# Performance work log

Measured on AMD Instinct MI355X. Metric: run time of the kernel, lower is better.

The kernel has to match this reference:

```python
import jax, jax.numpy as jnp
import numpy as np


def setup_inputs() -> dict:
    key = jax.random.key(0)
    k1, k2, k3, k4 = jax.random.split(key, 4)
    B, S, d_in, d_out = 4, 2048, 1024, 1024
    x = jax.random.normal(k1, (B, S, d_in), dtype=jnp.float32)
    # torch nn.Linear weight is [d_out, d_in]; we store transposed [d_in, d_out]
    Wq = jax.random.normal(k2, (d_in, d_out), dtype=jnp.float32) * (1.0 / np.sqrt(d_in))
    Wk = jax.random.normal(k3, (d_in, d_out), dtype=jnp.float32) * (1.0 / np.sqrt(d_in))
    Wv = jax.random.normal(k4, (d_in, d_out), dtype=jnp.float32) * (1.0 / np.sqrt(d_in))
    return {"x": x, "Wq": Wq, "Wk": Wk, "Wv": Wv}


def reference(x, Wq, Wk, Wv):
    # x: [B, S, d_in]
    B, S, d_in = x.shape
    q = jnp.einsum("bsd,de->bse", x, Wq)
    k = jnp.einsum("bsd,de->bse", x, Wk)
    v = jnp.einsum("bsd,de->bse", x, Wv)
    scores = jnp.einsum("bqe,bke->bqk", q, k)  # [B, S, S]
    causal = jnp.triu(jnp.ones((S, S), dtype=bool), k=1)  # True above diagonal
    scores = jnp.where(causal[None, :, :], -jnp.inf, scores)
    # NOTE: original scales by sqrt(d_in), not sqrt(d_out)
    scale = jnp.asarray(1.0 / np.sqrt(d_in), dtype=scores.dtype)
    weights = jax.nn.softmax(scores * scale, axis=-1)
    # dropout p=0.0 -> identity
    return jnp.einsum("bqk,bke->bqe", weights, v)
```

## Files before the change

kernel.cpp:

```cpp
#include <hip/hip_runtime.h>
#include <hip/hip_bf16.h>

typedef __attribute__((ext_vector_type(8))) short short8;
typedef __attribute__((ext_vector_type(4))) short short4_t;
typedef __attribute__((ext_vector_type(4))) float f32x4;
typedef unsigned short ushort_t;

__device__ __forceinline__ ushort_t f2bf(float f) {
    union { __hip_bfloat16 h; ushort_t u; } c;
    c.h = __float2bfloat16(f);
    return c.u;
}

__device__ __forceinline__ void gload16(const ushort_t* g, ushort_t* l) {
    __builtin_amdgcn_global_load_lds(
        (const __attribute__((address_space(1))) void*)g,
        (__attribute__((address_space(3))) void*)l, 16, 0, 0);
}

__global__ __launch_bounds__(256) void k_prep(const float* __restrict__ x,
                                              const float* __restrict__ Wq,
                                              const float* __restrict__ Wk,
                                              const float* __restrict__ Wv,
                                              ushort_t* __restrict__ xb,
                                              ushort_t* __restrict__ Wqb,
                                              ushort_t* __restrict__ Wkb,
                                              ushort_t* __restrict__ Wvt) {
    const int bz = blockIdx.z;
    const int t = threadIdx.y * 32 + threadIdx.x;
    if (bz == 3) {
        size_t base = ((size_t)(blockIdx.y * 32 + blockIdx.x) * 256 + t) * 8;
#pragma unroll
        for (int p = 0; p < 4; ++p) {
            size_t idx = base + (size_t)p * 2097152;
            float4 a = *(const float4*)(x + idx);
            float4 b = *(const float4*)(x + idx + 4);
            short8 o;
            o[0] = (short)f2bf(a.x); o[1] = (short)f2bf(a.y);
            o[2] = (short)f2bf(a.z); o[3] = (short)f2bf(a.w);
            o[4] = (short)f2bf(b.x); o[5] = (short)f2bf(b.y);
            o[6] = (short)f2bf(b.z); o[7] = (short)f2bf(b.w);
            *(short8*)(xb + idx) = o;
        }
        return;
    }
    if (bz < 2) {
        const float* src = bz ? Wk : Wq;
        ushort_t* dst = bz ? Wkb : Wqb;
        size_t idx = ((size_t)(blockIdx.y * 32 + blockIdx.x) * 256 + t) * 4;
        float4 a = *(const float4*)(src + idx);
        short4_t o;
        o[0] = (short)f2bf(a.x); o[1] = (short)f2bf(a.y);
        o[2] = (short)f2bf(a.z); o[3] = (short)f2bf(a.w);
        *(short4_t*)(dst + idx) = o;
        return;
    }
    __shared__ float tile[32][33];
    int tx = threadIdx.x, ty = threadIdx.y;
    int d0 = blockIdx.y * 32, e0 = blockIdx.x * 32;
#pragma unroll
    for (int i = 0; i < 32; i += 8)
        tile[ty + i][tx] = Wv[(size_t)(d0 + ty + i) * 1024 + e0 + tx];
    __syncthreads();
#pragma unroll
    for (int i = 0; i < 32; i += 8)
        Wvt[(size_t)(e0 + ty + i) * 1024 + d0 + tx] = f2bf(tile[tx][ty + i]);
}

template <int MODE>
__global__ __launch_bounds__(256) void k_gemm(const ushort_t* __restrict__ Abase,
                                              const ushort_t* __restrict__ Bbase,
                                              void* __restrict__ Cbase,
                                              ushort_t* __restrict__ Vt) {
    int bm, bn, bz;
    const ushort_t* A;
    const ushort_t* B;
    if constexpr (MODE == 3) {
        bm = blockIdx.x; bn = blockIdx.y; bz = 0;
        A = Abase; B = Bbase;
    } else {
        bm = blockIdx.x; bn = blockIdx.y; bz = blockIdx.z;
        A = Abase;
        B = Bbase + (size_t)bz * 1048576;
    }
    const int lda = 1024, ldb = 1024, nk = 32;

    constexpr int SMEM_ELEMS = (MODE == 0) ? (128 * 130) : 8192;
    __shared__ ushort_t smem[SMEM_ELEMS];
    ushort_t* As = smem;
    ushort_t* Bs = smem + 4096;

    const int tid = threadIdx.x;
    const int l = tid & 63, wid = tid >> 6;
    const int wr = (wid >> 1) * 64, wc = (wid & 1) * 64;
    const int lr = l & 15, kc = (l >> 4) * 8;

    const int srow = tid >> 2, skb = (tid & 3) * 8;
    const ushort_t* ag = A + (size_t)(bm * 128 + srow) * lda + skb;
    const ushort_t* bg = B + (size_t)(bn * 128 + srow) * ldb + skb;
    const size_t a64 = (size_t)64 * lda, b64 = (size_t)64 * ldb;
    ushort_t* al = As + tid * 8;
    ushort_t* bl = Bs + tid * 8;

    f32x4 zero = {0.f, 0.f, 0.f, 0.f};
    f32x4 acc[4][4];
#pragma unroll
    for (int m = 0; m < 4; ++m)
#pragma unroll
        for (int n = 0; n < 4; ++n) acc[m][n] = zero;

    for (int ks = 0; ks < nk; ++ks) {
        __syncthreads();
        gload16(ag, al);
        gload16(ag + a64, al + 2048);
        gload16(bg, bl);
        gload16(bg + b64, bl + 2048);
        ag += 32; bg += 32;
        __syncthreads();

        short8 a[4], b[4];
#pragma unroll
        for (int m = 0; m < 4; ++m)
            a[m] = *(const short8*)&As[(wr + m * 16 + lr) * 32 + kc];
#pragma unroll
        for (int n = 0; n < 4; ++n)
            b[n] = *(const short8*)&Bs[(wc + n * 16 + lr) * 32 + kc];
#pragma unroll
        for (int m = 0; m < 4; ++m)
#pragma unroll
            for (int n = 0; n < 4; ++n)
                acc[m][n] = __builtin_amdgcn_mfma_f32_16x16x32_bf16(a[m], b[n], acc[m][n], 0, 0, 0);
    }

    const int rbase = (l >> 4) * 4;
    const int cbase = l & 15;

    if constexpr (MODE == 0) {
        if (bz == 1) {
            __syncthreads();
#pragma unroll
            for (int m = 0; m < 4; ++m)
#pragma unroll
                for (int n = 0; n < 4; ++n) {
                    int col = wc + n * 16 + cbase;
                    int row0 = wr + m * 16 + rbase;
#pragma unroll
                    for (int r = 0; r < 4; ++r)
                        smem[col * 130 + row0 + r] = f2bf(acc[m][n][r]);
                }
            __syncthreads();
            const int e = tid >> 1, jh = (tid & 1) * 64;
            const int b = bm >> 4, j0 = (bm * 128) & 2047;
            ushort_t* dst = Vt + (size_t)b * 2097152 +
                            (size_t)(bn * 128 + e) * 2048 + j0 + jh;
            const ushort_t* src = smem + e * 130 + jh;
#pragma unroll
            for (int c = 0; c < 8; ++c)
                *(short8*)(dst + c * 8) = *(const short8*)(src + c * 8);
            return;
        }
    }

#pragma unroll
    for (int m = 0; m < 4; ++m) {
#pragma unroll
        for (int n = 0; n < 4; ++n) {
            int col = wc + n * 16 + cbase;
            int gcol = bn * 128 + col;
#pragma unroll
            for (int r = 0; r < 4; ++r) {
                int grow = bm * 128 + wr + m * 16 + rbase + r;
                ushort_t* C = (ushort_t*)Cbase;
                C[(size_t)grow * 1024 + gcol] = f2bf(acc[m][n][r]);
            }
        }
    }
}

template <int MODE>
__global__ __launch_bounds__(256) void k_gemm64(const ushort_t* __restrict__ Abase,
                                                const ushort_t* __restrict__ Bbase,
                                                void* __restrict__ Cbase) {
    int bm, bn;
    const int bz = blockIdx.z;
    const ushort_t* A;
    const ushort_t* B;
    int lda, ldb, nk;
    if constexpr (MODE == 1) {
        int x = blockIdx.x;
        bm = (int)((sqrtf(4.f * x + 1.f) - 1.f) * 0.5f);
        while ((bm + 1) * (bm + 2) <= x) ++bm;
        while (bm * (bm + 1) > x) --bm;
        bn = x - bm * (bm + 1);
        A = Abase + (size_t)bz * 2048 * 1024; lda = 1024;
        B = Bbase + (size_t)bz * 2048 * 1024; ldb = 1024;
        nk = 32;
    } else {
        int xr = blockIdx.x;
        bm = (xr & 1) ? (15 - (xr >> 1)) : (xr >> 1);
        bn = blockIdx.y;
        A = Abase + (size_t)bz * 2048 * 2048; lda = 2048;
        B = Bbase + (size_t)bz * 1024 * 2048; ldb = 2048;
        nk = (bm + 1) * 4;
    }

    __shared__ ushort_t As[128 * 32];
    __shared__ ushort_t Bs[64 * 32];
    __shared__ float rsh[128];

    const int tid = threadIdx.x;
    const int l = tid & 63, wid = tid >> 6;
    const int wr = (wid >> 1) * 64, wc = (wid & 1) * 32;
    const int lr = l & 15, kc = (l >> 4) * 8;

    const int srow = tid >> 2, skb = (tid & 3) * 8;
    const ushort_t* ag = A + (size_t)(bm * 128 + srow) * lda + skb;
    const ushort_t* bg = B + (size_t)(bn * 64 + srow) * ldb + skb;
    const size_t a64 = (size_t)64 * lda;
    ushort_t* al = As + tid * 8;
    ushort_t* bl = Bs + tid * 8;

    f32x4 zero = {0.f, 0.f, 0.f, 0.f};
    f32x4 acc[4][2];
#pragma unroll
    for (int m = 0; m < 4; ++m) { acc[m][0] = zero; acc[m][1] = zero; }

    f32x4 rs[4];
    short8 ones;
#pragma unroll
    for (int e = 0; e < 8; ++e) ones[e] = (short)0x3F80;
#pragma unroll
    for (int m = 0; m < 4; ++m) rs[m] = zero;

    for (int ks = 0; ks < nk; ++ks) {
        __syncthreads();
        gload16(ag, al);
        gload16(ag + a64, al + 2048);
        gload16(bg, bl);
        ag += 32; bg += 32;
        __syncthreads();

        short8 a[4], b[2];
#pragma unroll
        for (int m = 0; m < 4; ++m)
            a[m] = *(const short8*)&As[(wr + m * 16 + lr) * 32 + kc];
#pragma unroll
        for (int n = 0; n < 2; ++n)
            b[n] = *(const short8*)&Bs[(wc + n * 16 + lr) * 32 + kc];
#pragma unroll
        for (int m = 0; m < 4; ++m)
#pragma unroll
            for (int n = 0; n < 2; ++n)
                acc[m][n] = __builtin_amdgcn_mfma_f32_16x16x32_bf16(a[m], b[n], acc[m][n], 0, 0, 0);
        if constexpr (MODE == 2) {
            if (wc == 0) {
#pragma unroll
                for (int m = 0; m < 4; ++m)
                    rs[m] = __builtin_amdgcn_mfma_f32_16x16x32_bf16(a[m], ones, rs[m], 0, 0, 0);
            }
        }
    }

    const int rbase = (l >> 4) * 4;
    const int cbase = l & 15;

    if constexpr (MODE == 1) {
        ushort_t* C = (ushort_t*)Cbase + (size_t)bz * 2048 * 2048;
#pragma unroll
        for (int m = 0; m < 4; ++m)
#pragma unroll
            for (int n = 0; n < 2; ++n) {
                int gcol = bn * 64 + wc + n * 16 + cbase;
#pragma unroll
                for (int r = 0; r < 4; ++r) {
                    int grow = bm * 128 + wr + m * 16 + rbase + r;
                    ushort_t pv = (gcol <= grow) ? f2bf(__expf(acc[m][n][r] * 0.03125f))
                                                 : (ushort_t)0;
                    C[(size_t)grow * 2048 + gcol] = pv;
                }
            }
    } else {
        if (wc == 0 && lr == 0) {
#pragma unroll
            for (int m = 0; m < 4; ++m)
#pragma unroll
                for (int r = 0; r < 4; ++r)
                    rsh[wr + m * 16 + rbase + r] = rs[m][r];
        }
        __syncthreads();
        float inv[4][4];
#pragma unroll
        for (int m = 0; m < 4; ++m)
#pragma unroll
            for (int r = 0; r < 4; ++r)
                inv[m][r] = 1.0f / rsh[wr + m * 16 + rbase + r];
        float* C = (float*)Cbase + (size_t)bz * 2048 * 1024;
#pragma unroll
        for (int m = 0; m < 4; ++m)
#pragma unroll
            for (int n = 0; n < 2; ++n) {
                int gcol = bn * 64 + wc + n * 16 + cbase;
#pragma unroll
                for (int r = 0; r < 4; ++r) {
                    int grow = bm * 128 + wr + m * 16 + rbase + r;
                    C[(size_t)grow * 1024 + gcol] = acc[m][n][r] * inv[m][r];
                }
            }
    }
}

extern "C" void kernel_launch(void* const* d_in, const int* in_sizes, int n_in,
                              void* d_out, int out_size, void* d_ws, size_t ws_size,
                              hipStream_t stream) {
    const float* x  = (const float*)d_in[0];
    const float* Wq = (const float*)d_in[1];
    const float* Wk = (const float*)d_in[2];
    const float* Wv = (const float*)d_in[3];

    char* ws = (char*)d_ws;
    ushort_t* xb  = (ushort_t*)(ws);
    ushort_t* Wqb = (ushort_t*)(ws + 16777216);
    ushort_t* Wkb = (ushort_t*)(ws + 18874368);
    ushort_t* Mt  = (ushort_t*)(ws + 20971520);
    ushort_t* Wvt = (ushort_t*)(ws + 23068672);
    ushort_t* y   = (ushort_t*)(ws + 25165824);
    ushort_t* Vt  = (ushort_t*)(ws + 41943040);
    ushort_t* P   = (ushort_t*)(ws + 58720256);

    k_prep<<<dim3(32, 32, 4), dim3(32, 8), 0, stream>>>(x, Wq, Wk, Wv, xb, Wqb, Wkb, Wvt);
    k_gemm<3><<<dim3(8, 8), 256, 0, stream>>>(Wkb, Wqb, Mt, nullptr);
    k_gemm<0><<<dim3(64, 8, 2), 256, 0, stream>>>(xb, Mt, y, Vt);
    k_gemm64<1><<<dim3(272, 1, 4), 256, 0, stream>>>(y, xb, P);
    k_gemm64<2><<<dim3(16, 16, 4), 256, 0, stream>>>(P, Vt, (float*)d_out);
}
```

Measured before the change: 188.5 us.

## Widen attention GEMM tiles to 128x128 and double-buffer LDS loads

The two attention GEMM kernels (scores→exp and P·V) move from 128x64 tiles to 128x128 tiles, which halves the block count and doubles B-operand reuse per A load. The K loop now double-buffers LDS with a prefetch of the next stage before the MFMAs, so it needs one barrier per iteration instead of two. The row-sum MFMA now runs in every wave, and the reciprocal comes straight from registers instead of shared memory. In exchange the kernels use more registers and LDS, which can lower occupancy, and the causal triangle grid becomes coarser with fewer blocks to spread over the CUs.

After: 175.1 us. 7.1% less time.

```diff
diff --git a/kernel.cpp b/kernel.cpp
--- a/kernel.cpp
+++ b/kernel.cpp
@@ -178,9 +178,9 @@
 }
 
 template <int MODE>
-__global__ __launch_bounds__(256) void k_gemm64(const ushort_t* __restrict__ Abase,
-                                                const ushort_t* __restrict__ Bbase,
-                                                void* __restrict__ Cbase) {
+__global__ __launch_bounds__(256) void k_attn(const ushort_t* __restrict__ Abase,
+                                              const ushort_t* __restrict__ Bbase,
+                                              void* __restrict__ Cbase) {
     int bm, bn;
     const int bz = blockIdx.z;
     const ushort_t* A;
@@ -188,10 +188,10 @@
     int lda, ldb, nk;
     if constexpr (MODE == 1) {
         int x = blockIdx.x;
-        bm = (int)((sqrtf(4.f * x + 1.f) - 1.f) * 0.5f);
-        while ((bm + 1) * (bm + 2) <= x) ++bm;
-        while (bm * (bm + 1) > x) --bm;
-        bn = x - bm * (bm + 1);
+        bm = (int)((sqrtf(8.f * x + 1.f) - 1.f) * 0.5f);
+        while ((bm + 1) * (bm + 2) / 2 <= x) ++bm;
+        while (bm * (bm + 1) / 2 > x) --bm;
+        bn = x - bm * (bm + 1) / 2;
         A = Abase + (size_t)bz * 2048 * 1024; lda = 1024;
         B = Bbase + (size_t)bz * 2048 * 1024; ldb = 1024;
         nk = 32;
@@ -204,26 +204,25 @@
         nk = (bm + 1) * 4;
     }
 
-    __shared__ ushort_t As[128 * 32];
-    __shared__ ushort_t Bs[64 * 32];
-    __shared__ float rsh[128];
+    __shared__ ushort_t As[2][4096];
+    __shared__ ushort_t Bs[2][4096];
 
     const int tid = threadIdx.x;
     const int l = tid & 63, wid = tid >> 6;
-    const int wr = (wid >> 1) * 64, wc = (wid & 1) * 32;
+    const int wr = (wid >> 1) * 64, wc = (wid & 1) * 64;
     const int lr = l & 15, kc = (l >> 4) * 8;
 
     const int srow = tid >> 2, skb = (tid & 3) * 8;
     const ushort_t* ag = A + (size_t)(bm * 128 + srow) * lda + skb;
-    const ushort_t* bg = B + (size_t)(bn * 64 + srow) * ldb + skb;
-    const size_t a64 = (size_t)64 * lda;
-    ushort_t* al = As + tid * 8;
-    ushort_t* bl = Bs + tid * 8;
+    const ushort_t* bg = B + (size_t)(bn * 128 + srow) * ldb + skb;
+    const size_t a64 = (size_t)64 * lda, b64 = (size_t)64 * ldb;
 
     f32x4 zero = {0.f, 0.f, 0.f, 0.f};
-    f32x4 acc[4][2];
-#pragma unroll
-    for (int m = 0; m < 4; ++m) { acc[m][0] = zero; acc[m][1] = zero; }
+    f32x4 acc[4][4];
+#pragma unroll
+    for (int m = 0; m < 4; ++m)
+#pragma unroll
+        for (int n = 0; n < 4; ++n) acc[m][n] = zero;
 
     f32x4 rs[4];
     short8 ones;
@@ -232,33 +231,44 @@
 #pragma unroll
     for (int m = 0; m < 4; ++m) rs[m] = zero;
 
+    gload16(ag, &As[0][tid * 8]);
+    gload16(ag + a64, &As[0][tid * 8 + 2048]);
+    gload16(bg, &Bs[0][tid * 8]);
+    gload16(bg + b64, &Bs[0][tid * 8 + 2048]);
+    ag += 32; bg += 32;
+    __syncthreads();
+
+    int cur = 0;
     for (int ks = 0; ks < nk; ++ks) {
-        __syncthreads();
-        gload16(ag, al);
-        gload16(ag + a64, al + 2048);
-        gload16(bg, bl);
-        ag += 32; bg += 32;
-        __syncthreads();
-
-        short8 a[4], b[2];
-#pragma unroll
-        for (int m = 0; m < 4; ++m)
-            a[m] = *(const short8*)&As[(wr + m * 16 + lr) * 32 + kc];
-#pragma unroll
-        for (int n = 0; n < 2; ++n)
-            b[n] = *(const short8*)&Bs[(wc + n * 16 + lr) * 32 + kc];
-#pragma unroll
-        for (int m = 0; m < 4; ++m)
-#pragma unroll
-            for (int n = 0; n < 2; ++n)
+        if (ks + 1 < nk) {
+            const int nxt = cur ^ 1;
+            gload16(ag, &As[nxt][tid * 8]);
+            gload16(ag + a64, &As[nxt][tid * 8 + 2048]);
+            gload16(bg, &Bs[nxt][tid * 8]);
+            gload16(bg + b64, &Bs[nxt][tid * 8 + 2048]);
+            ag += 32; bg += 32;
+        }
+
+        short8 a[4], b[4];
+#pragma unroll
+        for (int m = 0; m < 4; ++m)
+            a[m] = *(const short8*)&As[cur][(wr + m * 16 + lr) * 32 + kc];
+#pragma unroll
+        for (int n = 0; n < 4; ++n)
+            b[n] = *(const short8*)&Bs[cur][(wc + n * 16 + lr) * 32 + kc];
+#pragma unroll
+        for (int m = 0; m < 4; ++m)
+#pragma unroll
+            for (int n = 0; n < 4; ++n)
                 acc[m][n] = __builtin_amdgcn_mfma_f32_16x16x32_bf16(a[m], b[n], acc[m][n], 0, 0, 0);
         if constexpr (MODE == 2) {
-            if (wc == 0) {
-#pragma unroll
-                for (int m = 0; m < 4; ++m)
-                    rs[m] = __builtin_amdgcn_mfma_f32_16x16x32_bf16(a[m], ones, rs[m], 0, 0, 0);
-            }
-        }
+#pragma unroll
+            for (int m = 0; m < 4; ++m)
+                rs[m] = __builtin_amdgcn_mfma_f32_16x16x32_bf16(a[m], ones, rs[m], 0, 0, 0);
+        }
+
+        __syncthreads();
+        cur ^= 1;
     }
 
     const int rbase = (l >> 4) * 4;
@@ -269,8 +279,8 @@
 #pragma unroll
         for (int m = 0; m < 4; ++m)
 #pragma unroll
-            for (int n = 0; n < 2; ++n) {
-                int gcol = bn * 64 + wc + n * 16 + cbase;
+            for (int n = 0; n < 4; ++n) {
+                int gcol = bn * 128 + wc + n * 16 + cbase;
 #pragma unroll
                 for (int r = 0; r < 4; ++r) {
                     int grow = bm * 128 + wr + m * 16 + rbase + r;
@@ -280,26 +290,17 @@
                 }
             }
     } else {
-        if (wc == 0 && lr == 0) {
-#pragma unroll
-            for (int m = 0; m < 4; ++m)
-#pragma unroll
-                for (int r = 0; r < 4; ++r)
-                    rsh[wr + m * 16 + rbase + r] = rs[m][r];
-        }
-        __syncthreads();
         float inv[4][4];
 #pragma unroll
         for (int m = 0; m < 4; ++m)
 #pragma unroll
-            for (int r = 0; r < 4; ++r)
-                inv[m][r] = 1.0f / rsh[wr + m * 16 + rbase + r];
+            for (int r = 0; r < 4; ++r) inv[m][r] = 1.0f / rs[m][r];
         float* C = (float*)Cbase + (size_t)bz * 2048 * 1024;
 #pragma unroll
         for (int m = 0; m < 4; ++m)
 #pragma unroll
-            for (int n = 0; n < 2; ++n) {
-                int gcol = bn * 64 + wc + n * 16 + cbase;
+            for (int n = 0; n < 4; ++n) {
+                int gcol = bn * 128 + wc + n * 16 + cbase;
 #pragma unroll
                 for (int r = 0; r < 4; ++r) {
                     int grow = bm * 128 + wr + m * 16 + rbase + r;
@@ -330,6 +331,6 @@
     k_prep<<<dim3(32, 32, 4), dim3(32, 8), 0, stream>>>(x, Wq, Wk, Wv, xb, Wqb, Wkb, Wvt);
     k_gemm<3><<<dim3(8, 8), 256, 0, stream>>>(Wkb, Wqb, Mt, nullptr);
     k_gemm<0><<<dim3(64, 8, 2), 256, 0, stream>>>(xb, Mt, y, Vt);
-    k_gemm64<1><<<dim3(272, 1, 4), 256, 0, stream>>>(y, xb, P);
-    k_gemm64<2><<<dim3(16, 16, 4), 256, 0, stream>>>(P, Vt, (float*)d_out);
-}
+    k_attn<1><<<dim3(136, 1, 4), 256, 0, stream>>>(y, xb, P);
+    k_attn<2><<<dim3(16, 8, 4), 256, 0, stream>>>(P, Vt, (float*)d_out);
+}
```
